# Performance work log

Measured on AMD Instinct MI355X. Metric: run time of the kernel, lower is better.

Reference implementation:

```python
import jax, jax.numpy as jnp
import numpy as np

NE = 14          # NUM_ELEMENTS
NC = 20          # NUM_CHANNEL
DEN = NE         # density channel
GRV = NE + 1     # gravity channel

# (id, density, gravity) per element, in id order
_ELEMS = [(0,1,1),(1,4,0),(2,3,1),(3,2,1),(4,0,1),(5,4,0),(6,4,0),(7,0,1),(8,4,0),(9,3,1),(10,3,1),(11,2,1),(12,3,1),(13,4,0)]

def _elem_table():
    t = np.zeros((NE, NC), dtype=np.float32)
    for eid, dens, grav in _ELEMS:
        t[eid, eid] = 1.0
        t[eid, DEN] = dens
        t[eid, GRV] = grav
    return jnp.asarray(t)

# torch.roll semantics: get_above(x)[h] = x[h-1] (wrap)
above = lambda x: jnp.roll(x, 1, axis=2)
below = lambda x: jnp.roll(x, -1, axis=2)
left  = lambda x: jnp.roll(x, 1, axis=3)
right = lambda x: jnp.roll(x, -1, axis=3)

def interp2(sa, sb, if_false, if_a, if_b):
    # faithful to torch: (~a & ~b)*f + a*xa + b*xb (bools broadcast-multiply floats)
    return (jnp.logical_and(~sa, ~sb)) * if_false + sa * if_a + sb * if_b

def setup_inputs() -> dict:
    key = jax.random.key(0)
    k1, k2 = jax.random.split(key)
    B, H, W = 8, 512, 512
    ids = jax.random.randint(k1, (B, H, W), 0, NE)
    world = _elem_table()[ids]                 # [B,H,W,NC]
    world = jnp.transpose(world, (0, 3, 1, 2)) # [B,NC,H,W]
    rand_movement = jax.random.uniform(k2, (B, 1, H, W), dtype=jnp.float32)
    return {"world": world, "rand_movement": rand_movement}

def reference(world, rand_movement):
    B, C, H, W = world.shape
    # --- stone support check (conv2d with zero padding, taps at top-left/top-right) ---
    stone = world[:, 9:10]
    p = jnp.pad(stone, ((0, 0), (0, 0), (1, 1), (1, 1)))
    supports = p[:, :, 0:H, 0:W] + p[:, :, 0:H, 2:W + 2]  # stone[h-1,w-1]+stone[h-1,w+1]
    new_grav = (1.0 - stone) * world[:, GRV:GRV + 1] + stone * (supports < 2)
    world = world.at[:, GRV:GRV + 1].set(new_grav)

    # --- vertical gravity passes over densities 0..3 ---
    did_gravity = jnp.zeros((B, 1, H, W), dtype=world.dtype)
    for curr_density in (0, 1, 2, 3):
        density = world[:, DEN:DEN + 1]
        is_density_above_greater = (above(density) - density) > 0
        is_density_below_less = below(is_density_above_greater)
        is_density_current = density == curr_density
        is_density_above_current = above(is_density_current)
        is_gravity = world[:, GRV:GRV + 1] == 1
        is_cb_gravity = jnp.logical_and(below(is_gravity), is_gravity)
        is_ca_gravity = jnp.logical_and(above(is_gravity), is_gravity)
        does_become_below = is_density_current & is_density_below_less & is_cb_gravity
        does_become_above = is_density_above_greater & is_density_above_current & is_ca_gravity
        did_gravity = did_gravity + does_become_above
        world = interp2(does_become_below, does_become_above, world, below(world), above(world))

    # --- diagonal fall for sand (2) and dust (12) ---
    for elem in (2, 12):
        fall_dir = rand_movement > 0.5
        not_did_gravity = did_gravity <= 0
        for fall_left in (True, False):
            g_dir = left if fall_left else right
            g_not = right if fall_left else left
            is_element = world[:, elem:elem + 1] == 1
            is_ar_element = g_not(above(is_element))
            density = world[:, DEN:DEN + 1]
            is_matching_fall = fall_dir if fall_left else ~fall_dir
            is_ar_matching_fall = g_not(above(is_matching_fall))
            is_bl_density_lower = (density - g_dir(below(density))) > 0
            is_ar_density_higher = (g_not(above(density)) - density) > 0
            is_gravity = world[:, GRV:GRV + 1] == 1
            is_bl_gravity = jnp.logical_and(g_dir(below(is_gravity)), is_gravity)
            is_ar_gravity = jnp.logical_and(g_not(above(is_gravity)), is_gravity)
            ndg_bl = jnp.logical_and(g_dir(below(not_did_gravity)), not_did_gravity)
            ndg_ar = jnp.logical_and(g_not(above(not_did_gravity)), not_did_gravity)
            does_become_bl = is_element & ndg_bl & is_matching_fall & is_bl_density_lower & is_bl_gravity
            does_become_ar = is_ar_element & ndg_ar & is_ar_matching_fall & is_ar_density_higher & is_ar_gravity
            world = interp2(does_become_bl, does_become_ar, world, g_dir(below(world)), g_not(above(world)))
    return world
```

## Files before the change

kernel.cpp:

```cpp
#include <hip/hip_runtime.h>
#include <stdint.h>

#define HH 512
#define WW 512
#define PLANE (HH*WW)
#define NCH 20

#define DENS_PACK 0x43233404402341ULL
#define GRAV_PACK 0x1E9Du

__device__ __forceinline__ int dens_of(int e) {
    return (int)((DENS_PACK >> (e * 4)) & 0xFULL);
}

__device__ __forceinline__ uint32_t eqz4(uint32_t x) {
    uint32_t nz = (x | (x >> 1) | (x >> 2) | (x >> 3)) & 0x01010101u;
    return nz ^ 0x01010101u;
}
__device__ __forceinline__ uint32_t gtb(uint32_t a, uint32_t b) {
    uint32_t t = (a | 0x08080808u) - b;
    return ((t + 0x07070707u) & 0x10101010u) >> 4;
}
__device__ __forceinline__ uint32_t bmask(uint32_t b) {
    uint32_t h = b << 7;
    return (h - (h >> 7)) | h;
}

__global__ __launch_bounds__(256) void extract_k(const float* __restrict__ world,
                                                 uint32_t* __restrict__ st) {
    int idx = blockIdx.x * 256 + threadIdx.x;
    int b  = idx >> 16;
    int p4 = idx & 0xFFFF;
    const float4* base = (const float4*)(world + (size_t)b * NCH * PLANE) + p4;
    int e0 = 0, e1 = 0, e2 = 0, e3 = 0;
#pragma unroll
    for (int c = 1; c < 14; ++c) {
        float4 v = base[c * (PLANE / 4)];
        if (v.x != 0.0f) e0 = c;
        if (v.y != 0.0f) e1 = c;
        if (v.z != 0.0f) e2 = c;
        if (v.w != 0.0f) e3 = c;
    }
#define PACK(e) ((uint32_t)((e) | (((GRAV_PACK >> (e)) & 1u) << 4) | (dens_of(e) << 5)))
    st[idx] = PACK(e0) | (PACK(e1) << 8) | (PACK(e2) << 16) | (PACK(e3) << 24);
#undef PACK
}

#define TILE 64
#define HALO_H 9
#define HALO_W 8
#define RH (TILE + 2*HALO_H)
#define RWW 20
#define RWS 21
#define NW (RH*RWW)

__global__ __launch_bounds__(512) void sim_k(const uint8_t* __restrict__ st_in,
                                             const float* __restrict__ rnd,
                                             float* __restrict__ out) {
    __shared__ uint32_t bufA[RH * RWS];
    __shared__ uint32_t bufB[RH * RWS];
    __shared__ uint32_t aux [RH * RWS];

    const int tid = threadIdx.x;
    const int b   = blockIdx.z;
    const int h0  = blockIdx.y * TILE;
    const int w0  = blockIdx.x * TILE;
    const uint8_t* stb = st_in + (size_t)b * PLANE;
    const float*   rb  = rnd   + (size_t)b * PLANE;

    for (int r = tid; r < NW; r += 512) {
        int i = r / RWW, jw = r - i * RWW;
        int gh  = (h0 + i - HALO_H) & (HH - 1);
        int gwb = (w0 + jw * 4 - HALO_W) & (WW - 1);
        bufA[i * RWS + jw] = *(const uint32_t*)(stb + gh * WW + gwb);
        const float* rp = rb + gh * WW + gwb;
        uint32_t aw = 0;
        aw |= (rp[0] > 0.5f) ? 0x00000001u : 0u;
        aw |= (rp[1] > 0.5f) ? 0x00000100u : 0u;
        aw |= (rp[2] > 0.5f) ? 0x00010000u : 0u;
        aw |= (rp[3] > 0.5f) ? 0x01000000u : 0u;
        aux[i * RWS + jw] = aw;
    }
    __syncthreads();

    for (int r = tid; r < NW; r += 512) {
        int i = r / RWW, jw = r - i * RWW;
        uint32_t s = bufA[i * RWS + jw];
        uint32_t stm = eqz4((s & 0x0F0F0F0Fu) ^ 0x09090909u);
        int im = (i > 0) ? i - 1 : 0;
        int jl = (jw > 0) ? jw - 1 : 0;
        int jr = (jw < RWW - 1) ? jw + 1 : RWW - 1;
        uint32_t wU  = bufA[im * RWS + jw];
        uint32_t wUL = bufA[im * RWS + jl];
        uint32_t wUR = bufA[im * RWS + jr];
        uint32_t upL = (wU << 8) | (wUL >> 24);
        uint32_t upR = (wU >> 8) | (wUR << 24);
        uint32_t stL = eqz4((upL & 0x0F0F0F0Fu) ^ 0x09090909u);
        uint32_t stR = eqz4((upR & 0x0F0F0F0Fu) ^ 0x09090909u);
        int gh  = (h0 + i - HALO_H) & (HH - 1);
        int gwb = (w0 + jw * 4 - HALO_W) & (WW - 1);
        uint32_t rowOK = (gh != 0) ? 0x01010101u : 0u;
        uint32_t okL = 0x01010101u ^ ((gwb == 0)      ? 0x00000001u : 0u);
        uint32_t okR = 0x01010101u ^ ((gwb == WW - 4) ? 0x01000000u : 0u);
        uint32_t supL = stL & okL & rowOK;
        uint32_t supR = stR & okR & rowOK;
        uint32_t g2 = 0x01010101u ^ (supL & supR);
        uint32_t ns = (s & ~0x10101010u) | (g2 << 4);
        bufB[i * RWS + jw] = s ^ ((s ^ ns) & bmask(stm));
    }
    __syncthreads();

    uint32_t* cur = bufB;
    uint32_t* nxt = bufA;

    for (int curr = 0; curr < 4; ++curr) {
        const uint32_t crep = (uint32_t)curr * 0x01010101u;
        for (int r = tid; r < NW; r += 512) {
            int i = r / RWW, jw = r - i * RWW;
            int ia = (i > 0) ? i - 1 : 0;
            int ib = (i < RH - 1) ? i + 1 : RH - 1;
            uint32_t s  = cur[i  * RWS + jw];
            uint32_t sa = cur[ia * RWS + jw];
            uint32_t sb = cur[ib * RWS + jw];
            uint32_t d  = (s  >> 5) & 0x07070707u;
            uint32_t da = (sa >> 5) & 0x07070707u;
            uint32_t db = (sb >> 5) & 0x07070707u;
            uint32_t g  = (s  >> 4) & 0x01010101u;
            uint32_t ga = (sa >> 4) & 0x01010101u;
            uint32_t gb = (sb >> 4) & 0x01010101u;
            uint32_t bel = eqz4(d ^ crep)  & gtb(d, db)  & gb & g;
            uint32_t abv = eqz4(da ^ crep) & gtb(da, d)  & ga & g;
            nxt[i * RWS + jw] = s ^ ((s ^ sb) & bmask(bel)) ^ ((s ^ sa) & bmask(abv));
            aux[i * RWS + jw] |= (abv << 1);
        }
        __syncthreads();
        uint32_t* t = cur; cur = nxt; nxt = t;
    }

    for (int pass = 0; pass < 4; ++pass) {
        const int  elem = (pass < 2) ? 2 : 12;
        const bool fl   = ((pass & 1) == 0);
        const uint32_t erep = (uint32_t)elem * 0x01010101u;
        for (int r = tid; r < NW; r += 512) {
            int i = r / RWW, jw = r - i * RWW;
            int ia = (i > 0) ? i - 1 : 0;
            int ib = (i < RH - 1) ? i + 1 : RH - 1;
            int jl = (jw > 0) ? jw - 1 : 0;
            int jr = (jw < RWW - 1) ? jw + 1 : RWW - 1;
            uint32_t s   = cur[i * RWS + jw];
            uint32_t wB  = cur[ib * RWS + jw];
            uint32_t wA  = cur[ia * RWS + jw];
            uint32_t aB  = aux[ib * RWS + jw];
            uint32_t aA  = aux[ia * RWS + jw];
            uint32_t sbl, sar, abl, aar;
            if (fl) {
                uint32_t wBL = cur[ib * RWS + jl], wAR = cur[ia * RWS + jr];
                uint32_t aBL = aux[ib * RWS + jl], aAR = aux[ia * RWS + jr];
                sbl = (wB << 8) | (wBL >> 24);
                sar = (wA >> 8) | (wAR << 24);
                abl = (aB << 8) | (aBL >> 24);
                aar = (aA >> 8) | (aAR << 24);
            } else {
                uint32_t wBR = cur[ib * RWS + jr], wAL = cur[ia * RWS + jl];
                uint32_t aBR = aux[ib * RWS + jr], aAL = aux[ia * RWS + jl];
                sbl = (wB >> 8) | (wBR << 24);
                sar = (wA << 8) | (wAL >> 24);
                abl = (aB >> 8) | (aBR << 24);
                aar = (aA << 8) | (aAL >> 24);
            }
            uint32_t ax = aux[i * RWS + jw];
            uint32_t d   = (s   >> 5) & 0x07070707u;
            uint32_t dbl = (sbl >> 5) & 0x07070707u;
            uint32_t dar = (sar >> 5) & 0x07070707u;
            uint32_t g   = (s   >> 4) & 0x01010101u;
            uint32_t gbl = (sbl >> 4) & 0x01010101u;
            uint32_t gar = (sar >> 4) & 0x01010101u;
            uint32_t ndg   = ((~ax)  >> 1) & 0x01010101u;
            uint32_t ndgbl = ((~abl) >> 1) & 0x01010101u;
            uint32_t ndgar = ((~aar) >> 1) & 0x01010101u;
            uint32_t mtc = (fl ? ax  : ~ax)  & 0x01010101u;
            uint32_t mta = (fl ? aar : ~aar) & 0x01010101u;
            uint32_t eqe  = eqz4((s   & 0x0F0F0F0Fu) ^ erep);
            uint32_t eqer = eqz4((sar & 0x0F0F0F0Fu) ^ erep);
            uint32_t bbl = eqe  & ndgbl & ndg & mtc & gtb(d, dbl)  & gbl & g;
            uint32_t bar = eqer & ndgar & ndg & mta & gtb(dar, d)  & gar & g;
            nxt[i * RWS + jw] = s ^ ((s ^ sbl) & bmask(bbl)) ^ ((s ^ sar) & bmask(bar));
        }
        __syncthreads();
        uint32_t* t = cur; cur = nxt; nxt = t;
    }

    float* ob = out + (size_t)b * NCH * PLANE;
    for (int idx = tid; idx < NCH * 64 * 16; idx += 512) {
        int col4 = idx & 15;
        int row  = (idx >> 4) & 63;
        int c    = idx >> 10;
        uint32_t w = cur[(HALO_H + row) * RWS + (HALO_W / 4) + col4];
        float4 v;
        float* vv = &v.x;
#pragma unroll
        for (int q = 0; q < 4; ++q) {
            uint32_t byte = (w >> (8 * q)) & 0xFFu;
            float val;
            if (c < 14)       val = ((byte & 15u) == (uint32_t)c) ? 1.0f : 0.0f;
            else if (c == 14) val = (float)((byte >> 5) & 7u);
            else if (c == 15) val = (float)((byte >> 4) & 1u);
            else              val = 0.0f;
            vv[q] = val;
        }
        *(float4*)(ob + (size_t)c * PLANE + (size_t)(h0 + row) * WW + (w0 + col4 * 4)) = v;
    }
}

extern "C" void kernel_launch(void* const* d_in, const int* in_sizes, int n_in,
                              void* d_out, int out_size, void* d_ws, size_t ws_size,
                              hipStream_t stream) {
    const float* world = (const float*)d_in[0];
    const float* rnd   = (const float*)d_in[1];
    float* out = (float*)d_out;
    uint32_t* st = (uint32_t*)d_ws;

    extract_k<<<2048, 256, 0, stream>>>(world, st);

    dim3 grid(WW / TILE, HH / TILE, 8);
    sim_k<<<grid, 512, 0, stream>>>((const uint8_t*)st, rnd, out);
}
```

Measured before the change: 64.13 us.

## Read fewer channels in extract, shrink sim tiles, vectorize random loads

The extract kernel now reads the density and gravity channels and uses density to narrow down the candidate element channels, so it loads 11 planes instead of 13. The simulation tile shrinks to 32 rows with 256 threads and an asymmetric halo (9 above, 8 below), and the random-field load becomes a single float4 read. The smaller tiles raise block count and occupancy but increase the share of halo work per block. The element decoding relies on density values matching the fixed element table, so it assumes well-formed inputs.

After: 62.90 us. About the same (-1.9%).

```diff
diff --git a/kernel.cpp b/kernel.cpp
--- a/kernel.cpp
+++ b/kernel.cpp
@@ -6,13 +6,6 @@
 #define PLANE (HH*WW)
 #define NCH 20
 
-#define DENS_PACK 0x43233404402341ULL
-#define GRAV_PACK 0x1E9Du
-
-__device__ __forceinline__ int dens_of(int e) {
-    return (int)((DENS_PACK >> (e * 4)) & 0xFULL);
-}
-
 __device__ __forceinline__ uint32_t eqz4(uint32_t x) {
     uint32_t nz = (x | (x >> 1) | (x >> 2) | (x >> 3)) & 0x01010101u;
     return nz ^ 0x01010101u;
@@ -24,6 +17,21 @@
 __device__ __forceinline__ uint32_t bmask(uint32_t b) {
     uint32_t h = b << 7;
     return (h - (h >> 7)) | h;
+}
+
+__device__ __forceinline__ uint32_t pack_cell(float d_, float g_,
+                                              float c1_, float c5_, float c6_, float c8_,
+                                              float c2_, float c9_, float c10_,
+                                              float c3_, float c4_) {
+    int d = (int)d_;
+    int e;
+    if (d == 4)      e = (c1_ != 0.f) ? 1 : (c5_ != 0.f) ? 5 : (c6_ != 0.f) ? 6 : (c8_ != 0.f) ? 8 : 13;
+    else if (d == 3) e = (c2_ != 0.f) ? 2 : (c9_ != 0.f) ? 9 : (c10_ != 0.f) ? 10 : 12;
+    else if (d == 2) e = (c3_ != 0.f) ? 3 : 11;
+    else if (d == 1) e = 0;
+    else             e = (c4_ != 0.f) ? 4 : 7;
+    int g = (g_ != 0.f) ? 1 : 0;
+    return (uint32_t)(e | (g << 4) | (d << 5));
 }
 
 __global__ __launch_bounds__(256) void extract_k(const float* __restrict__ world,
@@ -32,58 +40,64 @@
     int b  = idx >> 16;
     int p4 = idx & 0xFFFF;
     const float4* base = (const float4*)(world + (size_t)b * NCH * PLANE) + p4;
-    int e0 = 0, e1 = 0, e2 = 0, e3 = 0;
-#pragma unroll
-    for (int c = 1; c < 14; ++c) {
-        float4 v = base[c * (PLANE / 4)];
-        if (v.x != 0.0f) e0 = c;
-        if (v.y != 0.0f) e1 = c;
-        if (v.z != 0.0f) e2 = c;
-        if (v.w != 0.0f) e3 = c;
-    }
-#define PACK(e) ((uint32_t)((e) | (((GRAV_PACK >> (e)) & 1u) << 4) | (dens_of(e) << 5)))
-    st[idx] = PACK(e0) | (PACK(e1) << 8) | (PACK(e2) << 16) | (PACK(e3) << 24);
-#undef PACK
-}
-
-#define TILE 64
-#define HALO_H 9
+    float4 vD  = base[14 * (PLANE / 4)];
+    float4 vG  = base[15 * (PLANE / 4)];
+    float4 v1  = base[ 1 * (PLANE / 4)];
+    float4 v5  = base[ 5 * (PLANE / 4)];
+    float4 v6  = base[ 6 * (PLANE / 4)];
+    float4 v8  = base[ 8 * (PLANE / 4)];
+    float4 v2  = base[ 2 * (PLANE / 4)];
+    float4 v9  = base[ 9 * (PLANE / 4)];
+    float4 v10 = base[10 * (PLANE / 4)];
+    float4 v3  = base[ 3 * (PLANE / 4)];
+    float4 v4  = base[ 4 * (PLANE / 4)];
+    uint32_t b0 = pack_cell(vD.x, vG.x, v1.x, v5.x, v6.x, v8.x, v2.x, v9.x, v10.x, v3.x, v4.x);
+    uint32_t b1 = pack_cell(vD.y, vG.y, v1.y, v5.y, v6.y, v8.y, v2.y, v9.y, v10.y, v3.y, v4.y);
+    uint32_t b2 = pack_cell(vD.z, vG.z, v1.z, v5.z, v6.z, v8.z, v2.z, v9.z, v10.z, v3.z, v4.z);
+    uint32_t b3 = pack_cell(vD.w, vG.w, v1.w, v5.w, v6.w, v8.w, v2.w, v9.w, v10.w, v3.w, v4.w);
+    st[idx] = b0 | (b1 << 8) | (b2 << 16) | (b3 << 24);
+}
+
+#define TILE_R 32
+#define TILE_C 64
+#define HALO_T 9
+#define HALO_B 8
 #define HALO_W 8
-#define RH (TILE + 2*HALO_H)
+#define RH (TILE_R + HALO_T + HALO_B)
 #define RWW 20
 #define RWS 21
 #define NW (RH*RWW)
 
-__global__ __launch_bounds__(512) void sim_k(const uint8_t* __restrict__ st_in,
-                                             const float* __restrict__ rnd,
-                                             float* __restrict__ out) {
+__global__ __launch_bounds__(256, 4) void sim_k(const uint8_t* __restrict__ st_in,
+                                                const float* __restrict__ rnd,
+                                                float* __restrict__ out) {
     __shared__ uint32_t bufA[RH * RWS];
     __shared__ uint32_t bufB[RH * RWS];
     __shared__ uint32_t aux [RH * RWS];
 
     const int tid = threadIdx.x;
     const int b   = blockIdx.z;
-    const int h0  = blockIdx.y * TILE;
-    const int w0  = blockIdx.x * TILE;
+    const int h0  = blockIdx.y * TILE_R;
+    const int w0  = blockIdx.x * TILE_C;
     const uint8_t* stb = st_in + (size_t)b * PLANE;
     const float*   rb  = rnd   + (size_t)b * PLANE;
 
-    for (int r = tid; r < NW; r += 512) {
+    for (int r = tid; r < NW; r += 256) {
         int i = r / RWW, jw = r - i * RWW;
-        int gh  = (h0 + i - HALO_H) & (HH - 1);
+        int gh  = (h0 + i - HALO_T) & (HH - 1);
         int gwb = (w0 + jw * 4 - HALO_W) & (WW - 1);
         bufA[i * RWS + jw] = *(const uint32_t*)(stb + gh * WW + gwb);
-        const float* rp = rb + gh * WW + gwb;
+        float4 rv = *(const float4*)(rb + gh * WW + gwb);
         uint32_t aw = 0;
-        aw |= (rp[0] > 0.5f) ? 0x00000001u : 0u;
-        aw |= (rp[1] > 0.5f) ? 0x00000100u : 0u;
-        aw |= (rp[2] > 0.5f) ? 0x00010000u : 0u;
-        aw |= (rp[3] > 0.5f) ? 0x01000000u : 0u;
+        aw |= (rv.x > 0.5f) ? 0x00000001u : 0u;
+        aw |= (rv.y > 0.5f) ? 0x00000100u : 0u;
+        aw |= (rv.z > 0.5f) ? 0x00010000u : 0u;
+        aw |= (rv.w > 0.5f) ? 0x01000000u : 0u;
         aux[i * RWS + jw] = aw;
     }
     __syncthreads();
 
-    for (int r = tid; r < NW; r += 512) {
+    for (int r = tid; r < NW; r += 256) {
         int i = r / RWW, jw = r - i * RWW;
         uint32_t s = bufA[i * RWS + jw];
         uint32_t stm = eqz4((s & 0x0F0F0F0Fu) ^ 0x09090909u);
@@ -97,7 +111,7 @@
         uint32_t upR = (wU >> 8) | (wUR << 24);
         uint32_t stL = eqz4((upL & 0x0F0F0F0Fu) ^ 0x09090909u);
         uint32_t stR = eqz4((upR & 0x0F0F0F0Fu) ^ 0x09090909u);
-        int gh  = (h0 + i - HALO_H) & (HH - 1);
+        int gh  = (h0 + i - HALO_T) & (HH - 1);
         int gwb = (w0 + jw * 4 - HALO_W) & (WW - 1);
         uint32_t rowOK = (gh != 0) ? 0x01010101u : 0u;
         uint32_t okL = 0x01010101u ^ ((gwb == 0)      ? 0x00000001u : 0u);
@@ -115,7 +129,7 @@
 
     for (int curr = 0; curr < 4; ++curr) {
         const uint32_t crep = (uint32_t)curr * 0x01010101u;
-        for (int r = tid; r < NW; r += 512) {
+        for (int r = tid; r < NW; r += 256) {
             int i = r / RWW, jw = r - i * RWW;
             int ia = (i > 0) ? i - 1 : 0;
             int ib = (i < RH - 1) ? i + 1 : RH - 1;
@@ -141,7 +155,7 @@
         const int  elem = (pass < 2) ? 2 : 12;
         const bool fl   = ((pass & 1) == 0);
         const uint32_t erep = (uint32_t)elem * 0x01010101u;
-        for (int r = tid; r < NW; r += 512) {
+        for (int r = tid; r < NW; r += 256) {
             int i = r / RWW, jw = r - i * RWW;
             int ia = (i > 0) ? i - 1 : 0;
             int ib = (i < RH - 1) ? i + 1 : RH - 1;
@@ -191,11 +205,11 @@
     }
 
     float* ob = out + (size_t)b * NCH * PLANE;
-    for (int idx = tid; idx < NCH * 64 * 16; idx += 512) {
+    for (int idx = tid; idx < NCH * TILE_R * 16; idx += 256) {
         int col4 = idx & 15;
-        int row  = (idx >> 4) & 63;
-        int c    = idx >> 10;
-        uint32_t w = cur[(HALO_H + row) * RWS + (HALO_W / 4) + col4];
+        int row  = (idx >> 4) & (TILE_R - 1);
+        int c    = idx >> 9;
+        uint32_t w = cur[(HALO_T + row) * RWS + (HALO_W / 4) + col4];
         float4 v;
         float* vv = &v.x;
 #pragma unroll
@@ -222,6 +236,6 @@
 
     extract_k<<<2048, 256, 0, stream>>>(world, st);
 
-    dim3 grid(WW / TILE, HH / TILE, 8);
-    sim_k<<<grid, 512, 0, stream>>>((const uint8_t*)st, rnd, out);
-}
+    dim3 grid(WW / TILE_C, HH / TILE_R, 8);
+    sim_k<<<grid, 256, 0, stream>>>((const uint8_t*)st, rnd, out);
+}
```
